# Optimization experiments

Hardware: AMD Instinct MI355X
Metric: run time of the kernel (lower is better)

The kernel has to match this reference:

```python
import jax, jax.numpy as jnp
import numpy as np

NQ = 9  # 9 qubits per 3x3 patch; state shape (M, 2,...,2), axis (NQ-q) holds qubit q (qiskit little-endian)

def _ax(q):
    return NQ - q

def _bcast(theta):
    theta = jnp.asarray(theta)
    if theta.ndim == 1:  # per-patch angle -> broadcast over 8 remaining qubit axes
        return theta.reshape((-1,) + (1,) * (NQ - 1))
    return theta

def apply_1q(state, q, m00, m01, m10, m11):
    ax = _ax(q)
    s0 = jnp.take(state, 0, axis=ax)
    s1 = jnp.take(state, 1, axis=ax)
    return jnp.stack([m00 * s0 + m01 * s1, m10 * s0 + m11 * s1], axis=ax)

def apply_ry(state, q, theta):
    th = _bcast(theta) * 0.5
    c = jnp.cos(th).astype(state.dtype)
    s = jnp.sin(th).astype(state.dtype)
    return apply_1q(state, q, c, -s, s, c)

def apply_rz(state, q, theta):
    th = _bcast(theta) * 0.5
    e = jnp.exp(-1j * th.astype(jnp.complex64))
    return apply_1q(state, q, e, 0.0, 0.0, jnp.conj(e))

def apply_cx(state, c, t):
    axc, axt = _ax(c), _ax(t)
    sc0 = jnp.take(state, 0, axis=axc)
    sc1 = jnp.take(state, 1, axis=axc)
    axt2 = axt - 1 if axt > axc else axt
    sc1 = jnp.flip(sc1, axis=axt2)  # X on target within control=1 subspace
    return jnp.stack([sc0, sc1], axis=axc)

def apply_crx(state, c, t, theta):
    axc, axt = _ax(c), _ax(t)
    sc0 = jnp.take(state, 0, axis=axc)
    sc1 = jnp.take(state, 1, axis=axc)
    axt2 = axt - 1 if axt > axc else axt
    t0 = jnp.take(sc1, 0, axis=axt2)
    t1 = jnp.take(sc1, 1, axis=axt2)
    co = jnp.cos(theta * 0.5)
    si = jnp.sin(theta * 0.5)
    sc1 = jnp.stack([co * t0 - 1j * si * t1, -1j * si * t0 + co * t1], axis=axt2)
    return jnp.stack([sc0, sc1], axis=axc)

def qcnn_batched(angles, w):
    """angles: (M, 9) input rotation angles. w: (42,) shared weights. Returns (M, 3) = [<X>,<Y>,<Z>] on qubit 0."""
    M = angles.shape[0]
    state = jnp.zeros((M,) + (2,) * NQ, dtype=jnp.complex64)
    state = state.at[(slice(None),) + (0,) * NQ].set(1.0)
    for q in range(NQ):  # input encoding
        state = apply_ry(state, q, angles[:, q])
    wi = 0
    # conv1: RY + RZ on all 9 qubits, ring CNOT
    for q in range(NQ):
        state = apply_ry(state, q, w[wi]); wi += 1
    for q in range(NQ):
        state = apply_rz(state, q, w[wi]); wi += 1
    for i in range(NQ):
        state = apply_cx(state, i, (i + 1) % NQ)
    # pool1: 6 CRX gates
    for (c, t) in [(1, 0), (2, 0), (4, 3), (5, 3), (7, 6), (8, 6)]:
        state = apply_crx(state, c, t, w[wi]); wi += 1
    # conv2 on qubits [0,3,6]
    for q in [0, 3, 6]:
        state = apply_ry(state, q, w[wi]); wi += 1
    for q in [0, 3, 6]:
        state = apply_rz(state, q, w[wi]); wi += 1
    for (c, t) in [(0, 3), (3, 6), (6, 0)]:
        state = apply_cx(state, c, t)
    state = apply_ry(state, 0, w[wi])
    state = apply_rz(state, 3, w[wi + 1]); wi += 2
    # pool2
    state = apply_crx(state, 3, 0, w[wi])
    state = apply_crx(state, 3, 6, w[wi + 1])
    state = apply_ry(state, 0, w[wi + 2])
    state = apply_ry(state, 6, w[wi + 3]); wi += 4
    # conv3
    state = apply_ry(state, 0, w[wi])
    state = apply_ry(state, 6, w[wi + 1])
    state = apply_cx(state, 0, 6)
    state = apply_rz(state, 0, w[wi + 2])
    state = apply_rz(state, 6, w[wi + 3]); wi += 4
    # pool3
    state = apply_crx(state, 6, 0, w[wi])
    state = apply_ry(state, 0, w[wi + 1]); wi += 2
    assert wi == 42
    # expectations <X>,<Y>,<Z> on qubit 0 (last axis)
    a0 = jnp.take(state, 0, axis=NQ)
    a1 = jnp.take(state, 1, axis=NQ)
    axes = tuple(range(1, NQ))
    z = jnp.sum(jnp.conj(a0) * a1, axis=axes)
    ex = 2.0 * jnp.real(z)
    ey = 2.0 * jnp.imag(z)
    ez = jnp.sum(jnp.abs(a0) ** 2 - jnp.abs(a1) ** 2, axis=axes)
    return jnp.stack([ex, ey, ez], axis=-1).astype(jnp.float32)

def setup_inputs() -> dict:
    key = jax.random.key(0)
    k1, k2, k3 = jax.random.split(key, 3)
    B, H, WS, NCLS = 8, 28, 3, 10
    n = H - WS + 1  # 26 patches per side
    x = jax.random.uniform(k1, (B, 1, H, H), dtype=jnp.float32)
    w = jax.random.normal(k2, (42,), dtype=jnp.float32)
    fc_w = jax.random.normal(k3, (NCLS, n * n * 3), dtype=jnp.float32) * 0.02
    fc_b = jnp.zeros((NCLS,), dtype=jnp.float32)
    return {"x": x, "w": w, "fc_w": fc_w, "fc_b": fc_b}

def reference(x, w, fc_w, fc_b):
    B, H, WS = x.shape[0], x.shape[2], 3
    n = H - WS + 1
    # extract 3x3 patches, row-major within window (matches torch unfold+view)
    patches = jnp.stack([x[:, 0, i:i + n, j:j + n] for i in range(WS) for j in range(WS)], axis=-1)  # (B,n,n,9)
    angles = patches.reshape(B * n * n, WS * WS) * jnp.pi
    bloch = qcnn_batched(angles, w)  # (B*N, 3)
    feats = bloch.reshape(B, n * n * 3)  # patch-major [X,Y,Z] per patch, matches torch.cat over patches
    return feats @ fc_w.T + fc_b
```

## Files before the change

kernel.cpp:

```cpp
#include <hip/hip_runtime.h>


__device__ __forceinline__ float shx(float v, int m) { return __shfl_xor(v, m, 64); }

template <int TM> __device__ __forceinline__
void ry_r(float (&re)[8], float (&im)[8], float c, float s) {
#pragma unroll
  for (int r0 = 0; r0 < 8; ++r0) if (!(r0 & TM)) {
    const int r1 = r0 | TM;
    float a = re[r0], bb = re[r1];
    re[r0] = c * a - s * bb; re[r1] = s * a + c * bb;
    a = im[r0]; bb = im[r1];
    im[r0] = c * a - s * bb; im[r1] = s * a + c * bb;
  }
}

template <int TM> __device__ __forceinline__
void rz_r(float (&re)[8], float (&im)[8], float c, float s) {
#pragma unroll
  for (int r = 0; r < 8; ++r) {
    const float sg = (r & TM) ? s : -s;
    const float a = re[r], bb = im[r];
    re[r] = c * a - sg * bb;
    im[r] = c * bb + sg * a;
  }
}

template <int CM, int TM> __device__ __forceinline__
void cx_rr(float (&re)[8], float (&im)[8]) {
#pragma unroll
  for (int r0 = 0; r0 < 8; ++r0) if ((r0 & CM) && !(r0 & TM)) {
    const int r1 = r0 | TM;
    float t = re[r0]; re[r0] = re[r1]; re[r1] = t;
    t = im[r0]; im[r0] = im[r1]; im[r1] = t;
  }
}

template <int CL, int TM> __device__ __forceinline__
void cx_lr(float (&re)[8], float (&im)[8], int lane) {
  const bool ctl = (lane & CL) != 0;
#pragma unroll
  for (int r0 = 0; r0 < 8; ++r0) if (!(r0 & TM)) {
    const int r1 = r0 | TM;
    float a0 = re[r0], a1 = re[r1];
    re[r0] = ctl ? a1 : a0; re[r1] = ctl ? a0 : a1;
    a0 = im[r0]; a1 = im[r1];
    im[r0] = ctl ? a1 : a0; im[r1] = ctl ? a0 : a1;
  }
}

template <int CM, int TL> __device__ __forceinline__
void cx_rl(float (&re)[8], float (&im)[8]) {
#pragma unroll
  for (int r = 0; r < 8; ++r) if (r & CM) {
    re[r] = shx(re[r], TL);
    im[r] = shx(im[r], TL);
  }
}

template <int CL, int TL> __device__ __forceinline__
void cx_ll(float (&re)[8], float (&im)[8], int lane) {
  const bool ctl = (lane & CL) != 0;
#pragma unroll
  for (int r = 0; r < 8; ++r) {
    const float orr = shx(re[r], TL), oii = shx(im[r], TL);
    re[r] = ctl ? orr : re[r];
    im[r] = ctl ? oii : im[r];
  }
}

template <int CL, int TM> __device__ __forceinline__
void crx_lr(float (&re)[8], float (&im)[8], int lane, float co, float si) {
  const bool ctl = (lane & CL) != 0;
#pragma unroll
  for (int r0 = 0; r0 < 8; ++r0) if (!(r0 & TM)) {
    const int r1 = r0 | TM;
    const float r0r = re[r0], r0i = im[r0], r1r = re[r1], r1i = im[r1];
    const float n0r = co * r0r + si * r1i, n0i = co * r0i - si * r1r;
    const float n1r = co * r1r + si * r0i, n1i = co * r1i - si * r0r;
    re[r0] = ctl ? n0r : r0r; im[r0] = ctl ? n0i : r0i;
    re[r1] = ctl ? n1r : r1r; im[r1] = ctl ? n1i : r1i;
  }
}

template <int CM, int TM> __device__ __forceinline__
void crx_rr(float (&re)[8], float (&im)[8], float co, float si) {
#pragma unroll
  for (int r0 = 0; r0 < 8; ++r0) if ((r0 & CM) && !(r0 & TM)) {
    const int r1 = r0 | TM;
    const float r0r = re[r0], r0i = im[r0], r1r = re[r1], r1i = im[r1];
    re[r0] = co * r0r + si * r1i; im[r0] = co * r0i - si * r1r;
    re[r1] = co * r1r + si * r0i; im[r1] = co * r1i - si * r0r;
  }
}

__device__ __forceinline__ float fsel(int c, float a, float b) { return c ? a : b; }

__global__ __launch_bounds__(256) void qcnn_fused(const float* __restrict__ x,
                                                  const float* __restrict__ w,
                                                  float* __restrict__ feats) {
  __shared__ float  wenc[9];
  __shared__ float  wrzl[6];
  __shared__ float2 rztab[8];
  __shared__ float2 g[24];

  const int tid = threadIdx.x;
  if (tid < 9) {
    wenc[tid] = w[tid];
  } else if (tid < 15) {
    const int qmap[6] = {1, 2, 4, 5, 7, 8};
    wrzl[tid - 9] = 0.5f * w[9 + qmap[tid - 9]];
  } else if (tid >= 16 && tid < 24) {
    const int r = tid - 16;
    const float ph = ((r & 1) ? 0.5f : -0.5f) * w[9]
                   + ((r & 2) ? 0.5f : -0.5f) * w[12]
                   + ((r & 4) ? 0.5f : -0.5f) * w[15];
    float s, c; __sincosf(ph, &s, &c);
    rztab[r] = make_float2(c, s);
  } else if (tid >= 24 && tid < 48) {
    float s, c; __sincosf(0.5f * w[18 + tid - 24], &s, &c);
    g[tid - 24] = make_float2(c, s);
  }
  __syncthreads();

  const int lane = tid & 63;
  const unsigned p = blockIdx.x * 4u + (tid >> 6);
  const unsigned b = p / 676u;
  const unsigned rem = p - b * 676u;
  const unsigned i = rem / 26u, j = rem - i * 26u;
  const float* xb = x + b * 784u;

  float c_enc = 0.0f, s_enc = 0.0f;
  if (lane < 9) {
    const int di = lane / 3, dj = lane - di * 3;
    const float ang = fmaf(xb[(i + di) * 28u + (j + dj)],
                           3.14159265358979323846f, wenc[lane]) * 0.5f;
    __sincosf(ang, &s_enc, &c_enc);
  }
  float cq[9], sq[9];
#pragma unroll
  for (int q = 0; q < 9; ++q) { cq[q] = __shfl(c_enc, q, 64); sq[q] = __shfl(s_enc, q, 64); }

  float F = fsel(lane & 1,  sq[1], cq[1]);
  F      *= fsel(lane & 2,  sq[2], cq[2]);
  F      *= fsel(lane & 4,  sq[4], cq[4]);
  F      *= fsel(lane & 8,  sq[5], cq[5]);
  F      *= fsel(lane & 16, sq[7], cq[7]);
  F      *= fsel(lane & 32, sq[8], cq[8]);
  const float ph = (lane & 1  ? wrzl[0] : -wrzl[0])
                 + (lane & 2  ? wrzl[1] : -wrzl[1])
                 + (lane & 4  ? wrzl[2] : -wrzl[2])
                 + (lane & 8  ? wrzl[3] : -wrzl[3])
                 + (lane & 16 ? wrzl[4] : -wrzl[4])
                 + (lane & 32 ? wrzl[5] : -wrzl[5]);
  float sl, cl; __sincosf(ph, &sl, &cl);

  float re[8], im[8];
#pragma unroll
  for (int r = 0; r < 8; ++r) {
    const float pr = (r & 1 ? sq[0] : cq[0]) * (r & 2 ? sq[3] : cq[3]) * (r & 4 ? sq[6] : cq[6]);
    const float A = F * pr;
    const float cr = rztab[r].x, sr = rztab[r].y;
    const float cc = cl * cr - sl * sr;
    const float ss = sl * cr + cl * sr;
    re[r] = A * cc;
    im[r] = A * ss;
  }

  cx_rl<1, 1>(re, im);
  cx_ll<1, 2>(re, im, lane);
  cx_lr<2, 2>(re, im, lane);
  cx_rl<2, 4>(re, im);
  cx_ll<4, 8>(re, im, lane);
  cx_lr<8, 4>(re, im, lane);
  cx_rl<4, 16>(re, im);
  cx_ll<16, 32>(re, im, lane);
  cx_lr<32, 1>(re, im, lane);

  crx_lr<1,  1>(re, im, lane, g[0].x, g[0].y);
  crx_lr<2,  1>(re, im, lane, g[1].x, g[1].y);
  crx_lr<4,  2>(re, im, lane, g[2].x, g[2].y);
  crx_lr<8,  2>(re, im, lane, g[3].x, g[3].y);
  crx_lr<16, 4>(re, im, lane, g[4].x, g[4].y);
  crx_lr<32, 4>(re, im, lane, g[5].x, g[5].y);
  ry_r<1>(re, im, g[6].x, g[6].y);
  ry_r<2>(re, im, g[7].x, g[7].y);
  ry_r<4>(re, im, g[8].x, g[8].y);
  rz_r<1>(re, im, g[9].x, g[9].y);
  rz_r<2>(re, im, g[10].x, g[10].y);
  rz_r<4>(re, im, g[11].x, g[11].y);
  cx_rr<1, 2>(re, im);
  cx_rr<2, 4>(re, im);
  cx_rr<4, 1>(re, im);
  ry_r<1>(re, im, g[12].x, g[12].y);
  rz_r<2>(re, im, g[13].x, g[13].y);
  crx_rr<2, 1>(re, im, g[14].x, g[14].y);
  crx_rr<2, 4>(re, im, g[15].x, g[15].y);
  ry_r<1>(re, im, g[16].x, g[16].y);
  ry_r<4>(re, im, g[17].x, g[17].y);
  ry_r<1>(re, im, g[18].x, g[18].y);
  ry_r<4>(re, im, g[19].x, g[19].y);
  cx_rr<1, 4>(re, im);
  rz_r<1>(re, im, g[20].x, g[20].y);
  rz_r<4>(re, im, g[21].x, g[21].y);
  crx_rr<4, 1>(re, im, g[22].x, g[22].y);
  ry_r<1>(re, im, g[23].x, g[23].y);

  float zr = 0.f, zi = 0.f, ez = 0.f;
#pragma unroll
  for (int r0 = 0; r0 < 8; r0 += 2) {
    const int r1 = r0 + 1;
    zr += re[r0] * re[r1] + im[r0] * im[r1];
    zi += re[r0] * im[r1] - im[r0] * re[r1];
    ez += re[r0] * re[r0] + im[r0] * im[r0] - re[r1] * re[r1] - im[r1] * im[r1];
  }
#pragma unroll
  for (int m = 1; m < 64; m <<= 1) { zr += shx(zr, m); zi += shx(zi, m); ez += shx(ez, m); }

  if (lane == 0) {
    feats[p * 3u + 0u] = 2.0f * zr;
    feats[p * 3u + 1u] = 2.0f * zi;
    feats[p * 3u + 2u] = ez;
  }
}

__global__ __launch_bounds__(256) void fc_kernel(const float* __restrict__ feats,
                                                 const float* __restrict__ fc_w,
                                                 const float* __restrict__ fc_b,
                                                 float* __restrict__ out) {
  const int b = blockIdx.x / 10, c = blockIdx.x - b * 10;
  const float* f = feats + b * 2028;
  const float* wr = fc_w + c * 2028;
  float acc = 0.0f;
  for (int k = threadIdx.x; k < 2028; k += 256) acc += f[k] * wr[k];
#pragma unroll
  for (int m = 1; m < 64; m <<= 1) acc += __shfl_xor(acc, m, 64);
  __shared__ float sbuf[4];
  const int lane = threadIdx.x & 63, wv = threadIdx.x >> 6;
  if (lane == 0) sbuf[wv] = acc;
  __syncthreads();
  if (threadIdx.x == 0) out[b * 10 + c] = sbuf[0] + sbuf[1] + sbuf[2] + sbuf[3] + fc_b[c];
}

extern "C" void kernel_launch(void* const* d_in, const int* in_sizes, int n_in,
                              void* d_out, int out_size, void* d_ws, size_t ws_size,
                              hipStream_t stream) {
  const float* x    = (const float*)d_in[0];
  const float* w    = (const float*)d_in[1];
  const float* fc_w = (const float*)d_in[2];
  const float* fc_b = (const float*)d_in[3];
  float* out = (float*)d_out;

  const int B = in_sizes[0] / 784;
  const int npatch = B * 676;

  float* feats = (float*)d_ws;

  qcnn_fused<<<npatch / 4, 256, 0, stream>>>(x, w, feats);
  fc_kernel<<<B * 10, 256, 0, stream>>>(feats, fc_w, fc_b, out);
}
```

Measured before the change: 74.10 us.

## Precompute trailing 3-qubit unitary and merge lane-controlled CRX into per-lane RX

The per-patch tail of gates acting only on the three register qubits is input-independent, so eight threads now build the full 8x8 unitary once per block into shared memory. Each wave applies it as a dense complex matrix-vector product instead of replaying about twenty gates. The six lane-controlled CRX gates are folded into three per-lane RX rotations whose angles come from a small table indexed by lane bits. The Z expectation is computed from the qubit-0 probability using normalization. This adds a second block barrier and a 64-entry shared matrix read per wave, and the normalization shortcut assumes the state stays unit-norm in float precision.

```diff
diff --git a/kernel.cpp b/kernel.cpp
--- a/kernel.cpp
+++ b/kernel.cpp
@@ -2,6 +2,7 @@
 
 
 __device__ __forceinline__ float shx(float v, int m) { return __shfl_xor(v, m, 64); }
+__device__ __forceinline__ float fsel(int c, float a, float b) { return c ? a : b; }
 
 template <int TM> __device__ __forceinline__
 void ry_r(float (&re)[8], float (&im)[8], float c, float s) {
@@ -69,20 +70,6 @@
   }
 }
 
-template <int CL, int TM> __device__ __forceinline__
-void crx_lr(float (&re)[8], float (&im)[8], int lane, float co, float si) {
-  const bool ctl = (lane & CL) != 0;
-#pragma unroll
-  for (int r0 = 0; r0 < 8; ++r0) if (!(r0 & TM)) {
-    const int r1 = r0 | TM;
-    const float r0r = re[r0], r0i = im[r0], r1r = re[r1], r1i = im[r1];
-    const float n0r = co * r0r + si * r1i, n0i = co * r0i - si * r1r;
-    const float n1r = co * r1r + si * r0i, n1i = co * r1i - si * r0r;
-    re[r0] = ctl ? n0r : r0r; im[r0] = ctl ? n0i : r0i;
-    re[r1] = ctl ? n1r : r1r; im[r1] = ctl ? n1i : r1i;
-  }
-}
-
 template <int CM, int TM> __device__ __forceinline__
 void crx_rr(float (&re)[8], float (&im)[8], float co, float si) {
 #pragma unroll
@@ -94,7 +81,16 @@
   }
 }
 
-__device__ __forceinline__ float fsel(int c, float a, float b) { return c ? a : b; }
+template <int TM> __device__ __forceinline__
+void rx_l(float (&re)[8], float (&im)[8], float c, float s) {
+#pragma unroll
+  for (int r0 = 0; r0 < 8; ++r0) if (!(r0 & TM)) {
+    const int r1 = r0 | TM;
+    const float r0r = re[r0], r0i = im[r0], r1r = re[r1], r1i = im[r1];
+    re[r0] = c * r0r + s * r1i;  im[r0] = c * r0i - s * r1r;
+    re[r1] = c * r1r + s * r0i;  im[r1] = c * r1i - s * r0r;
+  }
+}
 
 __global__ __launch_bounds__(256) void qcnn_fused(const float* __restrict__ x,
                                                   const float* __restrict__ w,
@@ -103,6 +99,8 @@
   __shared__ float  wrzl[6];
   __shared__ float2 rztab[8];
   __shared__ float2 g[24];
+  __shared__ float2 rxtab[3][4];
+  __shared__ float2 Msh[8][8];
 
   const int tid = threadIdx.x;
   if (tid < 9) {
@@ -120,6 +118,44 @@
   } else if (tid >= 24 && tid < 48) {
     float s, c; __sincosf(0.5f * w[18 + tid - 24], &s, &c);
     g[tid - 24] = make_float2(c, s);
+  } else if (tid >= 48 && tid < 60) {
+    const int k = tid - 48, a = k >> 2, cb = k & 3;
+    float th = 0.0f;
+    if (cb & 1) th += w[18 + 2 * a];
+    if (cb & 2) th += w[19 + 2 * a];
+    float s, c; __sincosf(0.5f * th, &s, &c);
+    rxtab[a][cb] = make_float2(c, s);
+  }
+  __syncthreads();
+
+  if (tid < 8) {
+    float re[8], im[8];
+#pragma unroll
+    for (int r = 0; r < 8; ++r) { re[r] = (r == tid) ? 1.0f : 0.0f; im[r] = 0.0f; }
+    ry_r<1>(re, im, g[6].x, g[6].y);
+    ry_r<2>(re, im, g[7].x, g[7].y);
+    ry_r<4>(re, im, g[8].x, g[8].y);
+    rz_r<1>(re, im, g[9].x, g[9].y);
+    rz_r<2>(re, im, g[10].x, g[10].y);
+    rz_r<4>(re, im, g[11].x, g[11].y);
+    cx_rr<1, 2>(re, im);
+    cx_rr<2, 4>(re, im);
+    cx_rr<4, 1>(re, im);
+    ry_r<1>(re, im, g[12].x, g[12].y);
+    rz_r<2>(re, im, g[13].x, g[13].y);
+    crx_rr<2, 1>(re, im, g[14].x, g[14].y);
+    crx_rr<2, 4>(re, im, g[15].x, g[15].y);
+    ry_r<1>(re, im, g[16].x, g[16].y);
+    ry_r<4>(re, im, g[17].x, g[17].y);
+    ry_r<1>(re, im, g[18].x, g[18].y);
+    ry_r<4>(re, im, g[19].x, g[19].y);
+    cx_rr<1, 4>(re, im);
+    rz_r<1>(re, im, g[20].x, g[20].y);
+    rz_r<4>(re, im, g[21].x, g[21].y);
+    crx_rr<4, 1>(re, im, g[22].x, g[22].y);
+    ry_r<1>(re, im, g[23].x, g[23].y);
+#pragma unroll
+    for (int i = 0; i < 8; ++i) Msh[i][tid] = make_float2(re[i], im[i]);
   }
   __syncthreads();
 
@@ -177,50 +213,41 @@
   cx_ll<16, 32>(re, im, lane);
   cx_lr<32, 1>(re, im, lane);
 
-  crx_lr<1,  1>(re, im, lane, g[0].x, g[0].y);
-  crx_lr<2,  1>(re, im, lane, g[1].x, g[1].y);
-  crx_lr<4,  2>(re, im, lane, g[2].x, g[2].y);
-  crx_lr<8,  2>(re, im, lane, g[3].x, g[3].y);
-  crx_lr<16, 4>(re, im, lane, g[4].x, g[4].y);
-  crx_lr<32, 4>(re, im, lane, g[5].x, g[5].y);
-  ry_r<1>(re, im, g[6].x, g[6].y);
-  ry_r<2>(re, im, g[7].x, g[7].y);
-  ry_r<4>(re, im, g[8].x, g[8].y);
-  rz_r<1>(re, im, g[9].x, g[9].y);
-  rz_r<2>(re, im, g[10].x, g[10].y);
-  rz_r<4>(re, im, g[11].x, g[11].y);
-  cx_rr<1, 2>(re, im);
-  cx_rr<2, 4>(re, im);
-  cx_rr<4, 1>(re, im);
-  ry_r<1>(re, im, g[12].x, g[12].y);
-  rz_r<2>(re, im, g[13].x, g[13].y);
-  crx_rr<2, 1>(re, im, g[14].x, g[14].y);
-  crx_rr<2, 4>(re, im, g[15].x, g[15].y);
-  ry_r<1>(re, im, g[16].x, g[16].y);
-  ry_r<4>(re, im, g[17].x, g[17].y);
-  ry_r<1>(re, im, g[18].x, g[18].y);
-  ry_r<4>(re, im, g[19].x, g[19].y);
-  cx_rr<1, 4>(re, im);
-  rz_r<1>(re, im, g[20].x, g[20].y);
-  rz_r<4>(re, im, g[21].x, g[21].y);
-  crx_rr<4, 1>(re, im, g[22].x, g[22].y);
-  ry_r<1>(re, im, g[23].x, g[23].y);
-
-  float zr = 0.f, zi = 0.f, ez = 0.f;
+  const float2 x0 = rxtab[0][lane & 3];
+  const float2 x1 = rxtab[1][(lane >> 2) & 3];
+  const float2 x2 = rxtab[2][(lane >> 4) & 3];
+  rx_l<1>(re, im, x0.x, x0.y);
+  rx_l<2>(re, im, x1.x, x1.y);
+  rx_l<4>(re, im, x2.x, x2.y);
+
+  float nre[8], nim[8];
+#pragma unroll
+  for (int oi = 0; oi < 8; ++oi) {
+    float ar = 0.0f, ai = 0.0f;
+#pragma unroll
+    for (int jj = 0; jj < 8; ++jj) {
+      const float2 m = Msh[oi][jj];
+      ar = fmaf(m.x, re[jj], ar);  ar = fmaf(-m.y, im[jj], ar);
+      ai = fmaf(m.x, im[jj], ai);  ai = fmaf(m.y, re[jj], ai);
+    }
+    nre[oi] = ar; nim[oi] = ai;
+  }
+
+  float zr = 0.f, zi = 0.f, pe = 0.f;
 #pragma unroll
   for (int r0 = 0; r0 < 8; r0 += 2) {
     const int r1 = r0 + 1;
-    zr += re[r0] * re[r1] + im[r0] * im[r1];
-    zi += re[r0] * im[r1] - im[r0] * re[r1];
-    ez += re[r0] * re[r0] + im[r0] * im[r0] - re[r1] * re[r1] - im[r1] * im[r1];
-  }
-#pragma unroll
-  for (int m = 1; m < 64; m <<= 1) { zr += shx(zr, m); zi += shx(zi, m); ez += shx(ez, m); }
+    zr += nre[r0] * nre[r1] + nim[r0] * nim[r1];
+    zi += nre[r0] * nim[r1] - nim[r0] * nre[r1];
+    pe += nre[r0] * nre[r0] + nim[r0] * nim[r0];
+  }
+#pragma unroll
+  for (int m = 1; m < 64; m <<= 1) { zr += shx(zr, m); zi += shx(zi, m); pe += shx(pe, m); }
 
   if (lane == 0) {
     feats[p * 3u + 0u] = 2.0f * zr;
     feats[p * 3u + 1u] = 2.0f * zi;
-    feats[p * 3u + 2u] = ez;
+    feats[p * 3u + 2u] = 2.0f * pe - 1.0f;
   }
 }
 
```

After: 75.59 us. 2.0% more time.
